# Kernel tuning notes

Measured on AMD Instinct MI355X. Metric: run time of the kernel, lower is better.

Reference implementation:

```python
import jax, jax.numpy as jnp
import numpy as np
import math

N_LOC = 4096   # spatial locations
N_REP = 128    # replicates n
M_NBR = 48     # conditioning-set size m (fix_m = m_max)
SMOOTH = 1.5


def setup_inputs() -> dict:
    key = jax.random.key(0)
    k1, k2, k3, k4 = jax.random.split(key, 4)
    aug = jax.random.normal(k1, (N_REP, N_LOC, M_NBR + 1), dtype=jnp.float32)
    theta = jax.random.normal(k2, (6,), dtype=jnp.float32) * 0.1
    theta = theta.at[2].set(-2.5)  # slow scaling decay so m_max neighbors are all active
    scales = jax.random.uniform(k3, (N_LOC,), dtype=jnp.float32) + 0.5
    nug_mean = jax.random.uniform(k4, (N_LOC,), dtype=jnp.float32) + 0.5
    batch_idx = jnp.arange(N_LOC, dtype=jnp.int32)
    return {
        "augmented_response": aug,
        "theta": theta,
        "scales": scales,
        "nug_mean": nug_mean,
        "batch_idx": batch_idx,
    }


def _kernel(aug, theta, scales, nug_mean):
    m = aug.shape[-1] - 1
    # x: (n, N, m) -> (N, n, m), nan (no conditioning) -> 0
    x = aug[..., 1 : m + 1]
    x = jnp.where(jnp.isnan(x), 0.0, x)
    x = jnp.transpose(x, (1, 0, 2))  # (N, n, m)
    # scaling_fun(k) = sqrt(exp(-k * exp(theta[2]))), k = 1..m
    ks = jnp.arange(1, m + 1, dtype=aug.dtype)
    scal = jnp.sqrt(jnp.exp(-ks * jnp.exp(theta[2])))  # (m,)
    xs = x * scal  # (N, n, m)
    # linear term: per-location gram matrix (N, n, n)
    lin = jnp.einsum("Nim,Njm->Nij", xs, xs)
    # Matern-1.5 term with unit lengthscale on xs / lenScal
    len_scal = jnp.exp(theta[5]) * math.sqrt(2.0 * SMOOTH)
    xd = xs / len_scal
    sqn = jnp.sum(xd * xd, axis=-1)  # (N, n)
    sq = sqn[:, :, None] + sqn[:, None, :] - 2.0 * jnp.einsum("Nim,Njm->Nij", xd, xd)
    dist = jnp.sqrt(jnp.clip(sq, 0.0))
    sq3d = math.sqrt(3.0) * dist
    matern = (1.0 + sq3d) * jnp.exp(-sq3d)  # nu=1.5 Matern, lengthscale 1
    # sigma_fun per location: exp(log(scales) * theta[4] + theta[3])
    sigma = jnp.exp(jnp.log(scales) * theta[4] + theta[3])  # (N,)
    nonlin = (sigma**2)[:, None, None] * matern
    return (lin + nonlin) / nug_mean[:, None, None]


def reference(augmented_response, theta, scales, nug_mean, batch_idx):
    k = _kernel(augmented_response, theta, scales, nug_mean)  # (N, n, n)
    n = k.shape[-1]
    eye = jnp.eye(n, dtype=k.dtype)
    g = k + eye
    # locations with batch_idx == 0 get identity G
    g = jnp.where((batch_idx == 0)[:, None, None], eye, g)
    g_chol = jnp.linalg.cholesky(g)
    return g, g_chol
```

## Files before the change

kernel.cpp:

```cpp
#include <hip/hip_runtime.h>
#include <math.h>

#define NLOC 4096
#define NREP 128
#define MN   48
#define XTS  141
#define WLS  141

__device__ __forceinline__ int swz(int j) { return j + ((j >> 5) << 2); }

__device__ __forceinline__ float bcast(float v, int lane) {
    return __builtin_bit_cast(float,
        __builtin_amdgcn_readlane(__builtin_bit_cast(int, v), lane));
}

__global__ __launch_bounds__(256, 3)
void otm_fused(const float* __restrict__ aug,
               const float* __restrict__ theta,
               const float* __restrict__ scales,
               const float* __restrict__ nug_mean,
               const int*   __restrict__ batch_idx,
               float* __restrict__ out_g,
               float* __restrict__ out_l)
{
    __shared__ float smem_buf[MN * XTS];
    __shared__ float ldiag[NREP];
    __shared__ float scal_s[MN];
    __shared__ float rs_s[NREP];

    float* xs_t = smem_buf;
    typedef float wl_row[WLS];
    typedef wl_row wl_panel[8];
    wl_panel* wl = (wl_panel*)smem_buf;

    const int loc = blockIdx.x;
    const int tid = threadIdx.x;
    const int ti  = tid >> 4;
    const int tj  = tid & 15;
    const int i0  = ti << 3;
    const int j0  = tj << 3;
    const int sa  = swz(i0);
    const int sb  = swz(j0);

    const float th2 = theta[2];
    if (tid < MN) {
        float e2 = expf(th2);
        scal_s[tid] = expf(-0.5f * (float)(tid + 1) * e2);
    }
    __syncthreads();

    for (int idx = tid; idx < NREP * MN; idx += 256) {
        int r = idx / MN;
        int c = idx - r * MN;
        float v = aug[(r * NLOC + loc) * (MN + 1) + 1 + c];
        v = (v != v) ? 0.0f : v;
        xs_t[c * XTS + swz(r)] = v * scal_s[c];
    }
    __syncthreads();

    if (tid < NREP) {
        const int sr = swz(tid);
        float s = 0.0f;
        #pragma unroll
        for (int kk = 0; kk < MN; ++kk) {
            float v = xs_t[kk * XTS + sr];
            s = fmaf(v, v, s);
        }
        ldiag[tid] = s;
    }

    float acc[8][8];
    #pragma unroll
    for (int r = 0; r < 8; ++r)
        #pragma unroll
        for (int c = 0; c < 8; ++c) acc[r][c] = 0.0f;

    #pragma unroll 4
    for (int kk = 0; kk < MN; ++kk) {
        const float* row = &xs_t[kk * XTS];
        const float4 aA = *(const float4*)(row + sa);
        const float4 aB = *(const float4*)(row + sa + 4);
        const float4 bA = *(const float4*)(row + sb);
        const float4 bB = *(const float4*)(row + sb + 4);
        const float a[8] = {aA.x, aA.y, aA.z, aA.w, aB.x, aB.y, aB.z, aB.w};
        const float b[8] = {bA.x, bA.y, bA.z, bA.w, bB.x, bB.y, bB.z, bB.w};
        #pragma unroll
        for (int r = 0; r < 8; ++r)
            #pragma unroll
            for (int c = 0; c < 8; ++c)
                acc[r][c] = fmaf(a[r], b[c], acc[r][c]);
    }
    __syncthreads();

    const float s_loc   = scales[loc];
    const float th3 = theta[3], th4 = theta[4], th5 = theta[5];
    const float sig2    = expf(2.0f * fmaf(logf(s_loc), th4, th3));
    const float nug_inv = 1.0f / nug_mean[loc];
    const float ls      = expf(th5) * 1.7320508075688772f;
    const float inv_ls2 = 1.0f / (ls * ls);
    const bool  is0     = (batch_idx[loc] == 0);

    float di[8], dj[8];
    #pragma unroll
    for (int r = 0; r < 8; ++r) di[r] = ldiag[i0 + r];
    #pragma unroll
    for (int c = 0; c < 8; ++c) dj[c] = ldiag[j0 + c];

    float* gout = out_g + (size_t)loc * (NREP * NREP);
    #pragma unroll
    for (int r = 0; r < 8; ++r) {
        const int i = i0 + r;
        #pragma unroll
        for (int h = 0; h < 2; ++h) {
            float tmp[4];
            #pragma unroll
            for (int e = 0; e < 4; ++e) {
                const int c = h * 4 + e;
                const int j = j0 + c;
                float lin = acc[r][c];
                float sq  = (di[r] + dj[c] - 2.0f * lin) * inv_ls2;
                sq = fmaxf(sq, 0.0f);
                float d3  = 1.7320508075688772f * __builtin_amdgcn_sqrtf(sq);
                float mat = (1.0f + d3) * __expf(-d3);
                float gv  = fmaf(sig2, mat, lin) * nug_inv + ((i == j) ? 1.0f : 0.0f);
                if (is0) gv = (i == j) ? 1.0f : 0.0f;
                acc[r][c] = gv;
                tmp[e] = gv;
            }
            *(float4*)(gout + (size_t)i * NREP + j0 + h * 4) =
                make_float4(tmp[0], tmp[1], tmp[2], tmp[3]);
        }
    }

    for (int p = 0; p < 16; ++p) {
        if (ti == p && tj >= p) {
            const int diagLane = ((p & 3) << 4) | p;
            float rsv[8];
            #pragma unroll
            for (int s = 0; s < 8; ++s) {
                const float piv  = bcast(acc[s][s], diagLane);
                const float dinv = __builtin_amdgcn_rcpf(piv);
                rsv[s] = __builtin_amdgcn_rsqf(piv);
                #pragma unroll
                for (int sp = s + 1; sp < 8; ++sp) {
                    const float f = bcast(acc[sp][s], diagLane) * dinv;
                    #pragma unroll
                    for (int c = 0; c < 8; ++c) {
                        if (c > s) {
                            acc[sp][c] = fmaf(-f, acc[s][c], acc[sp][c]);
                        } else if (tj > p) {
                            acc[sp][c] = fmaf(-f, acc[s][c], acc[sp][c]);
                        }
                    }
                }
            }
            #pragma unroll
            for (int s = 0; s < 8; ++s) {
                *(float4*)&wl[p & 1][s][sb] =
                    make_float4(acc[s][0] * rsv[s], acc[s][1] * rsv[s],
                                acc[s][2] * rsv[s], acc[s][3] * rsv[s]);
                *(float4*)&wl[p & 1][s][sb + 4] =
                    make_float4(acc[s][4] * rsv[s], acc[s][5] * rsv[s],
                                acc[s][6] * rsv[s], acc[s][7] * rsv[s]);
            }
            if (tj == p) {
                #pragma unroll
                for (int s = 0; s < 8; ++s) rs_s[(p << 3) + s] = rsv[s];
            }
        }
        __syncthreads();

        if (ti > p) {
            const wl_row* w = wl[p & 1];
            if (tj > p) {
                #pragma unroll 2
                for (int s = 0; s < 8; ++s) {
                    const float4 wiA = *(const float4*)&w[s][sa];
                    const float4 wiB = *(const float4*)&w[s][sa + 4];
                    const float4 wjA = *(const float4*)&w[s][sb];
                    const float4 wjB = *(const float4*)&w[s][sb + 4];
                    const float wi[8] = {wiA.x, wiA.y, wiA.z, wiA.w,
                                         wiB.x, wiB.y, wiB.z, wiB.w};
                    const float wj[8] = {wjA.x, wjA.y, wjA.z, wjA.w,
                                         wjB.x, wjB.y, wjB.z, wjB.w};
                    #pragma unroll
                    for (int r = 0; r < 8; ++r)
                        #pragma unroll
                        for (int c = 0; c < 8; ++c)
                            acc[r][c] = fmaf(-wi[r], wj[c], acc[r][c]);
                }
            } else if (tj == p) {
                #pragma unroll
                for (int s = 0; s < 7; ++s) {
                    const float4 wiA = *(const float4*)&w[s][sa];
                    const float4 wiB = *(const float4*)&w[s][sa + 4];
                    const float wi[8] = {wiA.x, wiA.y, wiA.z, wiA.w,
                                         wiB.x, wiB.y, wiB.z, wiB.w};
                    #pragma unroll
                    for (int c = 0; c < 8; ++c) {
                        if (c > s) {
                            const float wjc = w[s][sb + c];
                            #pragma unroll
                            for (int r = 0; r < 8; ++r)
                                acc[r][c] = fmaf(-wi[r], wjc, acc[r][c]);
                        }
                    }
                }
            }
        }
    }

    float rsj[8];
    #pragma unroll
    for (int c = 0; c < 8; ++c) rsj[c] = rs_s[j0 + c];

    float* lout = out_l + (size_t)loc * (NREP * NREP);
    #pragma unroll
    for (int r = 0; r < 8; ++r) {
        const int i = i0 + r;
        #pragma unroll
        for (int h = 0; h < 2; ++h) {
            float tmp[4];
            #pragma unroll
            for (int e = 0; e < 4; ++e) {
                const int c = h * 4 + e;
                const int j = j0 + c;
                tmp[e] = (i >= j) ? acc[r][c] * rsj[c] : 0.0f;
            }
            *(float4*)(lout + (size_t)i * NREP + j0 + h * 4) =
                make_float4(tmp[0], tmp[1], tmp[2], tmp[3]);
        }
    }
}

extern "C" void kernel_launch(void* const* d_in, const int* in_sizes, int n_in,
                              void* d_out, int out_size, void* d_ws, size_t ws_size,
                              hipStream_t stream) {
    const float* aug    = (const float*)d_in[0];
    const float* theta  = (const float*)d_in[1];
    const float* scales = (const float*)d_in[2];
    const float* nug    = (const float*)d_in[3];
    const int*   bidx   = (const int*)d_in[4];
    float* g = (float*)d_out;
    float* l = g + (size_t)NLOC * NREP * NREP;
    hipLaunchKernelGGL(otm_fused, dim3(NLOC), dim3(256), 0, stream,
                       aug, theta, scales, nug, bidx, g, l);
}
```

Before: 1.144 ms.

## Remap row tiles across wavefronts and unify diagonal trailing update path

```diff
diff --git a/kernel.cpp b/kernel.cpp
--- a/kernel.cpp
+++ b/kernel.cpp
@@ -35,7 +35,7 @@
 
     const int loc = blockIdx.x;
     const int tid = threadIdx.x;
-    const int ti  = tid >> 4;
+    const int ti  = (((tid >> 4) & 3) << 2) | (tid >> 6);
     const int tj  = tid & 15;
     const int i0  = ti << 3;
     const int j0  = tj << 3;
@@ -134,7 +134,7 @@
 
     for (int p = 0; p < 16; ++p) {
         if (ti == p && tj >= p) {
-            const int diagLane = ((p & 3) << 4) | p;
+            const int diagLane = ((p >> 2) << 4) | (p & 15);
             float rsv[8];
             #pragma unroll
             for (int s = 0; s < 8; ++s) {
@@ -154,14 +154,19 @@
                     }
                 }
             }
+            const bool dz = (tj == p);
             #pragma unroll
             for (int s = 0; s < 8; ++s) {
+                float v[8];
+                #pragma unroll
+                for (int c = 0; c < 8; ++c) {
+                    float t = acc[s][c] * rsv[s];
+                    v[c] = (dz && (c <= s)) ? 0.0f : t;
+                }
                 *(float4*)&wl[p & 1][s][sb] =
-                    make_float4(acc[s][0] * rsv[s], acc[s][1] * rsv[s],
-                                acc[s][2] * rsv[s], acc[s][3] * rsv[s]);
+                    make_float4(v[0], v[1], v[2], v[3]);
                 *(float4*)&wl[p & 1][s][sb + 4] =
-                    make_float4(acc[s][4] * rsv[s], acc[s][5] * rsv[s],
-                                acc[s][6] * rsv[s], acc[s][7] * rsv[s]);
+                    make_float4(v[4], v[5], v[6], v[7]);
             }
             if (tj == p) {
                 #pragma unroll
@@ -172,7 +177,7 @@
 
         if (ti > p) {
             const wl_row* w = wl[p & 1];
-            if (tj > p) {
+            if (tj >= p) {
                 #pragma unroll 2
                 for (int s = 0; s < 8; ++s) {
                     const float4 wiA = *(const float4*)&w[s][sa];
@@ -189,23 +194,6 @@
                         for (int c = 0; c < 8; ++c)
                             acc[r][c] = fmaf(-wi[r], wj[c], acc[r][c]);
                 }
-            } else if (tj == p) {
-                #pragma unroll
-                for (int s = 0; s < 7; ++s) {
-                    const float4 wiA = *(const float4*)&w[s][sa];
-                    const float4 wiB = *(const float4*)&w[s][sa + 4];
-                    const float wi[8] = {wiA.x, wiA.y, wiA.z, wiA.w,
-                                         wiB.x, wiB.y, wiB.z, wiB.w};
-                    #pragma unroll
-                    for (int c = 0; c < 8; ++c) {
-                        if (c > s) {
-                            const float wjc = w[s][sb + c];
-                            #pragma unroll
-                            for (int r = 0; r < 8; ++r)
-                                acc[r][c] = fmaf(-wi[r], wjc, acc[r][c]);
-                        }
-                    }
-                }
             }
         }
     }
```

Measured after the change: 1.083 ms. -5.3%, faster.
